# Kernel tuning notes

Hardware: AMD Instinct MI355X
Metric: run time of the kernel (lower is better)

Reference implementation:

```python
import jax, jax.numpy as jnp
import numpy as np

B, C, H, W = 8, 512, 64, 64
HN = 8
HD = C // HN


def setup_inputs() -> dict:
    key = jax.random.key(0)
    ks = jax.random.split(key, 10)
    s = lambda k, shape: jax.random.normal(k, shape, jnp.float32) * 0.02
    return dict(
        x_opt=jax.random.normal(ks[0], (B, C, H, W), jnp.float32),
        x_sar=jax.random.normal(ks[1], (B, C, H, W), jnp.float32),
        ln_o_w=jnp.ones((C,), jnp.float32), ln_o_b=jnp.zeros((C,), jnp.float32),
        ln_s_w=jnp.ones((C,), jnp.float32), ln_s_b=jnp.zeros((C,), jnp.float32),
        wq=s(ks[2], (C, C)), bq=jnp.zeros((C,), jnp.float32),
        wk=s(ks[3], (C, C)), bk=jnp.zeros((C,), jnp.float32),
        wv=s(ks[4], (C, C)), bv=jnp.zeros((C,), jnp.float32),
        w1=s(ks[5], (C, 2 * C)), b1=jnp.zeros((2 * C,), jnp.float32),
        w2=s(ks[6], (2 * C, C)), b2=jnp.zeros((C,), jnp.float32),
        wo=s(ks[7], (C, C)), bo=jnp.zeros((C,), jnp.float32),
    )


def _ln2d(x, w, b, eps=1e-5):
    # LayerNorm over channel dim of [B,C,H,W]
    m = x.mean(axis=1, keepdims=True)
    v = x.var(axis=1, keepdims=True)
    return (x - m) / jnp.sqrt(v + eps) * w[None, :, None, None] + b[None, :, None, None]


def _conv1x1(x, w, b):
    # 1x1 conv == per-pixel channel matmul; w: [out,in]
    return jnp.einsum('bchw,dc->bdhw', x, w) + b[None, :, None, None]


def reference(x_opt, x_sar, ln_o_w, ln_o_b, ln_s_w, ln_s_b,
              wq, bq, wk, bk, wv, bv, w1, b1, w2, b2, wo, bo):
    Bb, Cc, Hh, Ww = x_opt.shape
    HW = Hh * Ww
    xo = _ln2d(x_opt, ln_o_w, ln_o_b)
    xs = _ln2d(x_sar, ln_s_w, ln_s_b)
    q = _conv1x1(xo, wq, bq).reshape(Bb, HN, HD, HW)
    k = _conv1x1(xs, wk, bk).reshape(Bb, HN, HD, HW)
    v = _conv1x1(xs, wv, bv).reshape(Bb, HN, HD, HW).transpose(0, 1, 3, 2)  # [B,HN,HW,HD]
    # L2-normalize over the spatial (HW) axis, F.normalize eps semantics
    q = q / jnp.maximum(jnp.linalg.norm(q, axis=-1, keepdims=True), 1e-12)
    k = k / jnp.maximum(jnp.linalg.norm(k, axis=-1, keepdims=True), 1e-12)
    # channel-channel attention in fp32: [B,HN,HD,HD]
    attn = jnp.einsum('bhdn,bhen->bhde', q.astype(jnp.float32), k.astype(jnp.float32)) * (HD ** -0.5)
    attn = (attn - attn.max(axis=-1, keepdims=True)).astype(q.dtype)
    attn = jax.nn.softmax(attn, axis=-1)
    z = jnp.einsum('bhnd,bhde->bhne', v, attn)  # [B,HN,HW,HD]
    z = z.transpose(0, 2, 1, 3).reshape(Bb, HW, Cc)
    z_opt = xo.reshape(Bb, Cc, HW).transpose(0, 2, 1)
    z_sum = z + z_opt
    h = jax.nn.gelu(z_sum @ w1 + b1, approximate=False) @ w2 + b2
    z_out = (h + z_sum).transpose(0, 2, 1).reshape(Bb, Cc, Hh, Ww)
    z_out = _conv1x1(z_out, wo, bo)
    return xo + z_out
```

## Files before the change

### kernel.cpp

```cpp
#include <hip/hip_runtime.h>
#include <cstdint>
#include <cstddef>

#define DEVI __device__ __forceinline__

typedef __attribute__((ext_vector_type(8))) short short8;
typedef __attribute__((ext_vector_type(4))) float f32x4;
typedef __attribute__((ext_vector_type(2))) unsigned short u16x2;
typedef __attribute__((ext_vector_type(4))) unsigned short u16x4;
typedef __attribute__((ext_vector_type(8))) unsigned short u16x8;

#define Bn 8
#define Cn 512
#define HWn 4096
#define Mtot 32768

DEVI float b2f(unsigned short u) {
  union { uint32_t u; float f; } c; c.u = ((uint32_t)u) << 16; return c.f;
}
DEVI unsigned short f2b(float f) {
  union { float f; uint32_t u; } c; c.f = f;
  uint32_t u = c.u + 0x7fffu + ((c.u >> 16) & 1u);
  return (unsigned short)(u >> 16);
}
DEVI float gelu_fast(float x) {
  float y = 0.7978845608f * (x + 0.044715f * x * x * x);
  float e = __expf(2.0f * y);
  float t = 1.0f - 2.0f / (e + 1.0f);
  return 0.5f * x * (1.0f + t);
}

DEVI void async16(const void* g, void* l) {
  __builtin_amdgcn_global_load_lds((const __attribute__((address_space(1))) uint32_t*)g,
                                   (__attribute__((address_space(3))) uint32_t*)l, 16, 0, 0);
}

DEVI void stage128(const unsigned short* __restrict__ src, int ld, int row0, int kt,
                   char* lds, int t) {
  const int w = t >> 6;
  const int srow = t >> 3, sph = t & 7;
#pragma unroll
  for (int i = 0; i < 4; ++i) {
    int row = i * 32 + srow;
    int slog = sph ^ (row & 7);
    async16(src + (size_t)(row0 + row) * ld + kt + slog * 8, lds + i * 4096 + w * 1024);
  }
}

DEVI void stage256(const unsigned short* __restrict__ src, int ld, int row0, int kt,
                   char* lds, int t) {
  const int w = t >> 6;
  const int srow = t >> 3, sph = t & 7;
#pragma unroll
  for (int i = 0; i < 4; ++i) {
    int row = i * 64 + srow;
    int slog = sph ^ (row & 7);
    async16(src + (size_t)(row0 + row) * ld + kt + slog * 8, lds + i * 8192 + w * 1024);
  }
}

DEVI void gemm_compute(const unsigned short* As, const unsigned short* Bs,
                       int wr, int wc, int l15, int l4, f32x4 (&acc)[4][4]) {
#pragma unroll
  for (int ks = 0; ks < 2; ++ks) {
    short8 af[4], bfv[4];
#pragma unroll
    for (int m = 0; m < 4; ++m) {
      int row = wr * 64 + m * 16 + l15;
      int slog = ks * 4 + l4;
      af[m] = *(const short8*)&As[row * 64 + ((slog ^ (row & 7)) << 3)];
    }
#pragma unroll
    for (int n = 0; n < 4; ++n) {
      int row = wc * 64 + n * 16 + l15;
      int slog = ks * 4 + l4;
      bfv[n] = *(const short8*)&Bs[row * 64 + ((slog ^ (row & 7)) << 3)];
    }
#pragma unroll
    for (int m = 0; m < 4; ++m)
#pragma unroll
      for (int n = 0; n < 4; ++n)
        acc[m][n] = __builtin_amdgcn_mfma_f32_16x16x32_bf16(af[m], bfv[n], acc[m][n], 0, 0, 0);
  }
}

__global__ __launch_bounds__(256, 4) void k_qkv(
    const unsigned short* __restrict__ XO, const unsigned short* __restrict__ XS,
    const unsigned short* __restrict__ WQKV,
    const float* __restrict__ bq, const float* __restrict__ bk, const float* __restrict__ bv,
    unsigned short* __restrict__ Qb, unsigned short* __restrict__ KVb,
    float* __restrict__ sqQ, float* __restrict__ sqK) {
  __shared__ __align__(16) char smem[33792];
  unsigned short* As = (unsigned short*)smem;
  unsigned short* Bs = (unsigned short*)(smem + 16384);
  const int lin = blockIdx.x + 12 * blockIdx.y;
  const int xcd = lin & 7, j = lin >> 3;
  const int mt = xcd * 32 + j / 12;
  const int nt = j % 12;
  const int m0 = mt * 128, n0 = nt * 128;
  const unsigned short* A = (nt < 4) ? XO : XS;
  const float* bb = (nt < 4) ? (bq + n0) : (nt < 8 ? (bk + (nt - 4) * 128) : (bv + (nt - 8) * 128));
  float* sq = (nt < 4) ? sqQ : (nt < 8 ? sqK : nullptr);
  const int scol0 = (nt < 4) ? n0 : (nt - 4) * 128;
  unsigned short* ob = (nt < 4) ? Qb : KVb;
  const int ldo = (nt < 4) ? 512 : 1024;
  const int oc0 = (nt < 4) ? n0 : (nt - 4) * 128;
  const int t = threadIdx.x, w = t >> 6, lane = t & 63;
  const int wr = w >> 1, wc = w & 1, l15 = lane & 15, l4 = lane >> 4;
  f32x4 acc[4][4] = {};

  for (int kt = 0; kt < 512; kt += 64) {
    stage128(A, 512, m0, kt, (char*)As, t);
    stage128(WQKV, 512, n0, kt, (char*)Bs, t);
    __syncthreads();
    gemm_compute(As, Bs, wr, wc, l15, l4, acc);
    __syncthreads();
  }

  unsigned short* Cs = (unsigned short*)smem;
#pragma unroll
  for (int n = 0; n < 4; ++n) {
    int cn = wc * 64 + n * 16 + l15;
    float bn = bb[cn];
    float s2 = 0.f;
#pragma unroll
    for (int m = 0; m < 4; ++m) {
      int rb = wr * 64 + m * 16 + l4 * 4;
#pragma unroll
      for (int q = 0; q < 4; ++q) {
        float v = acc[m][n][q] + bn;
        s2 += v * v;
        Cs[(rb + q) * 132 + cn] = f2b(v);
      }
    }
    if (sq) {
      s2 += __shfl_xor(s2, 16, 64);
      s2 += __shfl_xor(s2, 32, 64);
      if (l4 == 0) atomicAdd(&sq[(m0 >> 12) * Cn + scol0 + cn], s2);
    }
  }
  __syncthreads();
#pragma unroll
  for (int pass = 0; pass < 4; ++pass) {
    int r = pass * 32 + (t >> 3);
    int c = (t & 7) * 8;
    u16x8 v0 = *(const u16x8*)&Cs[r * 132 + c];
    u16x8 v1 = *(const u16x8*)&Cs[r * 132 + 64 + c];
    size_t base = (size_t)(m0 + r) * ldo + oc0;
    *(u16x8*)&ob[base + c] = v0;
    *(u16x8*)&ob[base + 64 + c] = v1;
  }
}

template <int MODE>
__global__ __launch_bounds__(256, 4) void k_ffn(
    const unsigned short* __restrict__ A, const unsigned short* __restrict__ W,
    const float* __restrict__ bias, const unsigned short* __restrict__ res,
    unsigned short* __restrict__ out, int K, int N) {
  __shared__ __align__(16) char smem[33792];
  unsigned short* As = (unsigned short*)smem;
  unsigned short* Bs = (unsigned short*)(smem + 16384);
  const int NT = gridDim.x;
  const int lin = blockIdx.x + NT * blockIdx.y;
  const int xcd = lin & 7, j = lin >> 3;
  const int mt = xcd * 32 + j / NT;
  const int nt = j % NT;
  const int m0 = mt * 128, n0 = nt * 128;
  const int t = threadIdx.x, w = t >> 6, lane = t & 63;
  const int wr = w >> 1, wc = w & 1, l15 = lane & 15, l4 = lane >> 4;
  f32x4 acc[4][4] = {};

  for (int kt = 0; kt < K; kt += 64) {
    stage128(A, K, m0, kt, (char*)As, t);
    stage128(W, K, n0, kt, (char*)Bs, t);
    __syncthreads();
    gemm_compute(As, Bs, wr, wc, l15, l4, acc);
    __syncthreads();
  }

  unsigned short* Cs = (unsigned short*)smem;
#pragma unroll
  for (int n = 0; n < 4; ++n) {
    int cn = wc * 64 + n * 16 + l15;
    float bn = bias[n0 + cn];
#pragma unroll
    for (int m = 0; m < 4; ++m) {
      int rb = wr * 64 + m * 16 + l4 * 4;
#pragma unroll
      for (int q = 0; q < 4; ++q) {
        float v = acc[m][n][q] + bn;
        if (MODE == 1) v = gelu_fast(v);
        Cs[(rb + q) * 132 + cn] = f2b(v);
      }
    }
  }
  __syncthreads();
#pragma unroll
  for (int pass = 0; pass < 4; ++pass) {
    int r = pass * 32 + (t >> 3);
    int c = (t & 7) * 8;
    u16x8 v0 = *(const u16x8*)&Cs[r * 132 + c];
    u16x8 v1 = *(const u16x8*)&Cs[r * 132 + 64 + c];
    size_t base = (size_t)(m0 + r) * N + n0;
    if (MODE == 2) {
      u16x8 r0 = *(const u16x8*)&res[base + c];
      u16x8 r1 = *(const u16x8*)&res[base + 64 + c];
#pragma unroll
      for (int jj = 0; jj < 8; ++jj) {
        v0[jj] = f2b(b2f(v0[jj]) + b2f(r0[jj]));
        v1[jj] = f2b(b2f(v1[jj]) + b2f(r1[jj]));
      }
    }
    *(u16x8*)&out[base + c] = v0;
    *(u16x8*)&out[base + 64 + c] = v1;
  }
}

DEVI void compute256(const unsigned short* Ab, const unsigned short* Bb,
                     int wr, int wc, int l15, int l4, f32x4 (&acc)[8][4]) {
#pragma unroll
  for (int ks = 0; ks < 2; ++ks) {
    short8 aF[8], bF[4];
#pragma unroll
    for (int mf = 0; mf < 8; ++mf) {
      int row = wr * 128 + mf * 16 + l15;
      aF[mf] = *(const short8*)&Ab[row * 64 + (((ks * 4 + l4) ^ (row & 7)) << 3)];
    }
#pragma unroll
    for (int nf = 0; nf < 4; ++nf) {
      int row = wc * 64 + nf * 16 + l15;
      bF[nf] = *(const short8*)&Bb[row * 64 + (((ks * 4 + l4) ^ (row & 7)) << 3)];
    }
#pragma unroll
    for (int mf = 0; mf < 8; ++mf)
#pragma unroll
      for (int nf = 0; nf < 4; ++nf)
        acc[mf][nf] = __builtin_amdgcn_mfma_f32_16x16x32_bf16(aF[mf], bF[nf], acc[mf][nf], 0, 0, 0);
  }
}

__global__ __launch_bounds__(512, 2) void k_gemm_out(
    const unsigned short* __restrict__ Wo, const unsigned short* __restrict__ U,
    const float* __restrict__ bo, const float* __restrict__ xopt,
    const float* __restrict__ meanG, const float* __restrict__ rstdG,
    const float* __restrict__ lnw, const float* __restrict__ lnb,
    float* __restrict__ out) {
  __shared__ __align__(16) char smem[131072];
  const int lin = blockIdx.x;
  const int xcd = lin & 7, j = lin >> 3;
  const int b = xcd, mt = j & 1, nt = j >> 1;
  const int m0 = mt * 256, n0 = nt * 256;
  const unsigned short* Ub = U + (size_t)b * HWn * Cn;
  const int t = threadIdx.x, lane = t & 63;
  const int w = t >> 6, wr = w >> 2, wc = w & 3;
  const int l15 = lane & 15, l4 = lane >> 4;
  f32x4 acc[8][4] = {};

  stage256(Wo, 512, m0, 0, smem, t);
  stage256(Ub, 512, n0, 0, smem + 32768, t);
  __syncthreads();
  for (int kt = 0; kt < 8; ++kt) {
    if (kt + 1 < 8) {
      char* nb = smem + ((kt + 1) & 1) * 65536;
      stage256(Wo, 512, m0, (kt + 1) * 64, nb, t);
      stage256(Ub, 512, n0, (kt + 1) * 64, nb + 32768, t);
    }
    const unsigned short* Ab = (const unsigned short*)(smem + (kt & 1) * 65536);
    const unsigned short* Bb = (const unsigned short*)(smem + (kt & 1) * 65536 + 32768);
    compute256(Ab, Bb, wr, wc, l15, l4, acc);
    __syncthreads();
  }

  float* Fs = (float*)smem;
#pragma unroll
  for (int qd = 0; qd < 4; ++qd) {
    __syncthreads();
    if (wr == (qd >> 1)) {
#pragma unroll
      for (int nf = 0; nf < 4; ++nf) {
        int cn = wc * 64 + nf * 16 + l15;
#pragma unroll
        for (int mf2 = 0; mf2 < 4; ++mf2) {
          int mf = (qd & 1) * 4 + mf2;
#pragma unroll
          for (int q = 0; q < 4; ++q)
            Fs[(mf2 * 16 + l4 * 4 + q) * 260 + cn] = acc[mf][nf][q];
        }
      }
    }
    __syncthreads();
#pragma unroll
    for (int p = 0; p < 8; ++p) {
      int cl = p * 8 + w;
      int px = lane * 4;
      int c = m0 + qd * 64 + cl;
      size_t gbase = (size_t)(b * Cn + c) * HWn + n0 + px;
      f32x4 z = *(const f32x4*)&Fs[cl * 260 + px];
      f32x4 xv = *(const f32x4*)&xopt[gbase];
      f32x4 mn4 = *(const f32x4*)&meanG[b * HWn + n0 + px];
      f32x4 rs4 = *(const f32x4*)&rstdG[b * HWn + n0 + px];
      float lw = lnw[c], lb = lnb[c], bc = bo[c];
      f32x4 o;
#pragma unroll
      for (int jj = 0; jj < 4; ++jj)
        o[jj] = z[jj] + bc + (xv[jj] - mn4[jj]) * rs4[jj] * lw + lb;
      *(f32x4*)&out[gbase] = o;
    }
  }
}

__global__ __launch_bounds__(256, 2) void k_z(
    const unsigned short* __restrict__ V, int ldv, const unsigned short* __restrict__ PT,
    const unsigned short* __restrict__ XO, unsigned short* __restrict__ ZS) {
  __shared__ __align__(16) char smem[24576];
  unsigned short* As = (unsigned short*)smem;
  unsigned short* Bs = (unsigned short*)(smem + 16384);
  const int mt = blockIdx.x, bh = blockIdx.y, b = bh >> 3, h = bh & 7;
  const int t = threadIdx.x, w = t >> 6, lane = t & 63;
  const int wr = w >> 1, wc = w & 1, l15 = lane & 15, l4 = lane >> 4;
  const int srow = t >> 3, sph = t & 7;
#pragma unroll
  for (int i = 0; i < 4; ++i) {
    int row = i * 32 + srow;
    int slog = sph ^ (row & 7);
    async16(V + (size_t)(b * HWn + mt * 128 + row) * ldv + h * 64 + slog * 8,
            (char*)As + i * 4096 + w * 1024);
  }
#pragma unroll
  for (int i = 0; i < 2; ++i) {
    int row = i * 32 + srow;
    int slog = sph ^ (row & 7);
    async16(PT + (size_t)bh * 4096 + row * 64 + slog * 8, (char*)Bs + i * 4096 + w * 1024);
  }
  __syncthreads();
  f32x4 acc[4][2] = {};
#pragma unroll
  for (int ks = 0; ks < 2; ++ks) {
    short8 af[4], bfv[2];
#pragma unroll
    for (int m = 0; m < 4; ++m) {
      int row = wr * 64 + m * 16 + l15;
      int slog = ks * 4 + l4;
      af[m] = *(const short8*)&As[row * 64 + ((slog ^ (row & 7)) << 3)];
    }
#pragma unroll
    for (int n = 0; n < 2; ++n) {
      int row = wc * 32 + n * 16 + l15;
      int slog = ks * 4 + l4;
      bfv[n] = *(const short8*)&Bs[row * 64 + ((slog ^ (row & 7)) << 3)];
    }
#pragma unroll
    for (int m = 0; m < 4; ++m)
#pragma unroll
      for (int n = 0; n < 2; ++n)
        acc[m][n] = __builtin_amdgcn_mfma_f32_16x16x32_bf16(af[m], bfv[n], acc[m][n], 0, 0, 0);
  }
  __syncthreads();
  unsigned short* Cs = (unsigned short*)smem;
#pragma unroll
  for (int n = 0; n < 2; ++n) {
    int e = wc * 32 + n * 16 + l15;
#pragma unroll
    for (int m = 0; m < 4; ++m) {
      int rb = wr * 64 + m * 16 + l4 * 4;
#pragma unroll
      for (int q = 0; q < 4; ++q) Cs[(rb + q) * 72 + e] = f2b(acc[m][n][q]);
    }
  }
  __syncthreads();
#pragma unroll
  for (int pass = 0; pass < 4; ++pass) {
    int r = pass * 32 + (t >> 3);
    int c = (t & 7) * 8;
    u16x8 v = *(const u16x8*)&Cs[r * 72 + c];
    size_t idx = (size_t)(b * HWn + mt * 128 + r) * Cn + h * 64 + c;
    u16x8 xo = *(const u16x8*)&XO[idx];
#pragma unroll
    for (int jj = 0; jj < 8; ++jj) v[jj] = f2b(b2f(v[jj]) + b2f(xo[jj]));
    *(u16x8*)&ZS[idx] = v;
  }
}

__global__ __launch_bounds__(256, 2) void k_ln(
    const float* __restrict__ x_opt, const float* __restrict__ x_sar,
    const float* __restrict__ lwo, const float* __restrict__ lbo,
    const float* __restrict__ lws, const float* __restrict__ lbs,
    unsigned short* __restrict__ XO, unsigned short* __restrict__ XS,
    float* __restrict__ meanG, float* __restrict__ rstdG) {
  const int zz = blockIdx.z;
  const float* x = zz ? x_sar : x_opt;
  const float* lw = zz ? lws : lwo;
  const float* lb = zz ? lbs : lbo;
  unsigned short* out = zz ? XS : XO;
  __shared__ unsigned short stash[512 * 34];
  __shared__ float redS[256 * 4], redQ[256 * 4];
  __shared__ float meanS[32], rstdS[32], wS[512], bS[512];
  const int b = blockIdx.y, n0 = blockIdx.x * 32;
  const int t = threadIdx.x;
  wS[t] = lw[t]; wS[t + 256] = lw[t + 256];
  bS[t] = lb[t]; bS[t + 256] = lb[t + 256];
  const int cg = t >> 3, pq = t & 7;
  float sum[4] = {}, sq[4] = {};
  for (int r = 0; r < 16; ++r) {
    int c = r * 32 + cg;
    f32x4 v = *(const f32x4*)(x + (size_t)(b * Cn + c) * HWn + n0 + pq * 4);
#pragma unroll
    for (int j = 0; j < 4; ++j) { sum[j] += v[j]; sq[j] += v[j] * v[j]; }
    u16x2 h0 = {f2b(v[0]), f2b(v[1])};
    u16x2 h1 = {f2b(v[2]), f2b(v[3])};
    *(u16x2*)&stash[c * 34 + pq * 4] = h0;
    *(u16x2*)&stash[c * 34 + pq * 4 + 2] = h1;
  }
#pragma unroll
  for (int j = 0; j < 4; ++j) { redS[t * 4 + j] = sum[j]; redQ[t * 4 + j] = sq[j]; }
  __syncthreads();
  if (t < 32) {
    float s = 0.f, qq = 0.f;
    int pqq = t >> 2, j = t & 3;
    for (int g = 0; g < 32; ++g) {
      s += redS[(g * 8 + pqq) * 4 + j];
      qq += redQ[(g * 8 + pqq) * 4 + j];
    }
    float mean = s * (1.0f / 512.0f);
    float var = qq * (1.0f / 512.0f) - mean * mean;
    float rstd = rsqrtf(var + 1e-5f);
    meanS[t] = mean; rstdS[t] = rstd;
    if (!zz) { meanG[b * HWn + n0 + t] = mean; rstdG[b * HWn + n0 + t] = rstd; }
  }
  __syncthreads();
  const int p = t >> 3, cs = t & 7;
  float mn = meanS[p], rs = rstdS[p];
  for (int ch = 0; ch < 4; ++ch) {
    u16x8 o0, o1;
#pragma unroll
    for (int j = 0; j < 16; ++j) {
      int c = ch * 128 + cs * 16 + j;
      float xv = b2f(stash[c * 34 + p]);
      unsigned short r2 = f2b((xv - mn) * rs * wS[c] + bS[c]);
      if (j < 8) o0[j] = r2; else o1[j - 8] = r2;
    }
    size_t base = (size_t)(b * HWn + n0 + p) * Cn + ch * 128 + cs * 16;
    *(u16x8*)&out[base] = o0;
    *(u16x8*)&out[base + 8] = o1;
  }
}

__global__ __launch_bounds__(256, 2) void k_attn_part(
    const unsigned short* __restrict__ Q, int ldq,
    const unsigned short* __restrict__ Kb, int ldk,
    float* __restrict__ Praw) {
  __shared__ __align__(16) unsigned short QT[64 * 136];
  __shared__ __align__(16) unsigned short KT[64 * 136];
  const int bh = blockIdx.x, ns = blockIdx.y, b = bh >> 3, h = bh & 7;
  const int t = threadIdx.x, w = t >> 6, lane = t & 63;
  const int l15 = lane & 15, l4 = lane >> 4;
  const int dh = w >> 1, eh = w & 1;
  const int c8 = t >> 5, rr = t & 31;
  f32x4 acc[2][2] = {};
  for (int chunk = 0; chunk < 4; ++chunk) {
    int n0 = ns * 512 + chunk * 128;
    __syncthreads();
#pragma unroll
    for (int pass = 0; pass < 2; ++pass) {
      int row = n0 + pass * 64 + 2 * rr;
      u16x8 q0 = *(const u16x8*)(Q + (size_t)(b * HWn + row) * ldq + h * 64 + c8 * 8);
      u16x8 q1 = *(const u16x8*)(Q + (size_t)(b * HWn + row + 1) * ldq + h * 64 + c8 * 8);
      u16x8 k0 = *(const u16x8*)(Kb + (size_t)(b * HWn + row) * ldk + h * 64 + c8 * 8);
      u16x8 k1 = *(const u16x8*)(Kb + (size_t)(b * HWn + row + 1) * ldk + h * 64 + c8 * 8);
#pragma unroll
      for (int j = 0; j < 8; ++j) {
        u16x2 pq = {q0[j], q1[j]};
        u16x2 pk = {k0[j], k1[j]};
        *(u16x2*)&QT[(c8 * 8 + j) * 136 + pass * 64 + 2 * rr] = pq;
        *(u16x2*)&KT[(c8 * 8 + j) * 136 + pass * 64 + 2 * rr] = pk;
      }
    }
    __syncthreads();
#pragma unroll
    for (int ks = 0; ks < 4; ++ks) {
      short8 af[2], bfv[2];
#pragma unroll
      for (int m = 0; m < 2; ++m)
        af[m] = *(const short8*)&QT[(dh * 32 + m * 16 + l15) * 136 + ks * 32 + l4 * 8];
#pragma unroll
      for (int n = 0; n < 2; ++n)
        bfv[n] = *(const short8*)&KT[(eh * 32 + n * 16 + l15) * 136 + ks * 32 + l4 * 8];
#pragma unroll
      for (int m = 0; m < 2; ++m)
#pragma unroll
        for (int n = 0; n < 2; ++n)
          acc[m][n] = __builtin_amdgcn_mfma_f32_16x16x32_bf16(af[m], bfv[n], acc[m][n], 0, 0, 0);
    }
  }
#pragma unroll
  for (int m = 0; m < 2; ++m)
#pragma unroll
    for (int n = 0; n < 2; ++n)
#pragma unroll
      for (int q = 0; q < 4; ++q) {
        int dd = dh * 32 + m * 16 + l4 * 4 + q;
        int ee = eh * 32 + n * 16 + l15;
        atomicAdd(&Praw[(size_t)bh * 4096 + dd * 64 + ee], acc[m][n][q]);
      }
}

__global__ __launch_bounds__(256, 2) void k_softmax(
    const float* __restrict__ Praw, const float* __restrict__ sqQ,
    const float* __restrict__ sqK, unsigned short* __restrict__ PT) {
  __shared__ float P3[64 * 66];
  const int bh = blockIdx.x, b = bh >> 3, h = bh & 7;
  const int t = threadIdx.x, w = t >> 6, lane = t & 63;
  float rk = 1.0f / fmaxf(sqrtf(sqK[b * Cn + h * 64 + lane]), 1e-12f);
  for (int i = 0; i < 16; ++i) {
    int d = w * 16 + i;
    float rqd = 1.0f / fmaxf(sqrtf(sqQ[b * Cn + h * 64 + d]), 1e-12f);
    float v = Praw[(size_t)bh * 4096 + d * 64 + lane] * (rqd * rk * 0.125f);
    float m = v;
    for (int o = 32; o > 0; o >>= 1) m = fmaxf(m, __shfl_xor(m, o, 64));
    float p = __expf(v - m);
    float s = p;
    for (int o = 32; o > 0; o >>= 1) s += __shfl_xor(s, o, 64);
    P3[lane * 66 + d] = p / s;
  }
  __syncthreads();
  {
    int e = t >> 2, dg = (t & 3) * 16;
    u16x8 o0, o1;
#pragma unroll
    for (int j = 0; j < 8; ++j) {
      o0[j] = f2b(P3[e * 66 + dg + j]);
      o1[j] = f2b(P3[e * 66 + dg + 8 + j]);
    }
    size_t base = (size_t)bh * 4096 + e * 64 + dg;
    *(u16x8*)&PT[base] = o0;
    *(u16x8*)&PT[base + 8] = o1;
  }
}

__global__ void k_prep(const float* __restrict__ wq, const float* __restrict__ wk,
                       const float* __restrict__ wv, const float* __restrict__ wo,
                       const float* __restrict__ w1, const float* __restrict__ w2,
                       unsigned short* __restrict__ WQKV, unsigned short* __restrict__ WO,
                       unsigned short* __restrict__ W1T, unsigned short* __restrict__ W2T) {
  int bid = blockIdx.x;
  if (bid < 1024) {
    const int mat = bid >> 8, chunk = bid & 255;
    const float* s = mat == 0 ? wq : mat == 1 ? wk : mat == 2 ? wv : wo;
    unsigned short* d = mat == 3 ? WO : (WQKV + mat * 262144);
    int idx = chunk * 1024 + threadIdx.x * 4;
    f32x4 v = *(const f32x4*)(s + idx);
    u16x4 o = {f2b(v[0]), f2b(v[1]), f2b(v[2]), f2b(v[3])};
    *(u16x4*)(d + idx) = o;
    return;
  }
  bid -= 1024;
  __shared__ float tile[32][33];
  const float* src; unsigned short* dst; int R, C, r0, c0;
  if (bid < 512) { src = w1; dst = W1T; R = 512; C = 1024; r0 = (bid >> 5) * 32; c0 = (bid & 31) * 32; }
  else { bid -= 512; src = w2; dst = W2T; R = 1024; C = 512; r0 = (bid >> 4) * 32; c0 = (bid & 15) * 32; }
  const int tx = threadIdx.x & 31, ty = threadIdx.x >> 5;
#pragma unroll
  for (int i = 0; i < 4; ++i)
    tile[ty + i * 8][tx] = src[(size_t)(r0 + ty + i * 8) * C + c0 + tx];
  __syncthreads();
#pragma unroll
  for (int i = 0; i < 4; ++i)
    dst[(size_t)(c0 + ty + i * 8) * R + r0 + tx] = f2b(tile[tx][ty + i * 8]);
}

extern "C" void kernel_launch(void* const* d_in, const int* in_sizes, int n_in,
                              void* d_out, int out_size, void* d_ws, size_t ws_size,
                              hipStream_t stream) {
  const float* x_opt = (const float*)d_in[0];
  const float* x_sar = (const float*)d_in[1];
  const float* ln_o_w = (const float*)d_in[2];
  const float* ln_o_b = (const float*)d_in[3];
  const float* ln_s_w = (const float*)d_in[4];
  const float* ln_s_b = (const float*)d_in[5];
  const float* wq = (const float*)d_in[6];
  const float* bq = (const float*)d_in[7];
  const float* wk = (const float*)d_in[8];
  const float* bk = (const float*)d_in[9];
  const float* wv = (const float*)d_in[10];
  const float* bv = (const float*)d_in[11];
  const float* w1 = (const float*)d_in[12];
  const float* b1 = (const float*)d_in[13];
  const float* w2 = (const float*)d_in[14];
  const float* b2 = (const float*)d_in[15];
  const float* wo = (const float*)d_in[16];
  const float* bo = (const float*)d_in[17];
  float* out = (float*)d_out;

  char* ws = (char*)d_ws;
  const size_t S = (size_t)Mtot * Cn * 2;
  unsigned short* XO = (unsigned short*)(ws);
  unsigned short* XS = (unsigned short*)(ws + S);
  unsigned short* Qb = (unsigned short*)(ws + 2 * S);
  unsigned short* KVb = (unsigned short*)(ws + 3 * S);
  unsigned short* ZS = (unsigned short*)(ws + 5 * S);
  unsigned short* H1 = Qb;
  unsigned short* Ub = XS;
  char* E = ws + 6 * S;
  unsigned short* PT = (unsigned short*)(E);
  float* Praw = (float*)(E + 524288);
  float* sqQ = (float*)(E + 524288 + 1048576);
  float* sqK = (float*)(E + 524288 + 1048576 + 16384);
  float* meanG = (float*)(E + 524288 + 1048576 + 32768);
  float* rstdG = (float*)(E + 524288 + 1048576 + 32768 + 131072);
  char* Wb = E + 1867776;
  unsigned short* WQKV = (unsigned short*)(Wb);
  unsigned short* WO = (unsigned short*)(Wb + 1572864);
  unsigned short* W1T = (unsigned short*)(Wb + 2097152);
  unsigned short* W2T = (unsigned short*)(Wb + 2097152 + 1048576);

  hipMemsetAsync(E + 524288, 0, 1048576 + 32768, stream);

  k_prep<<<2048, 256, 0, stream>>>(wq, wk, wv, wo, w1, w2, WQKV, WO, W1T, W2T);

  k_ln<<<dim3(128, Bn, 2), 256, 0, stream>>>(x_opt, x_sar, ln_o_w, ln_o_b, ln_s_w, ln_s_b,
                                             XO, XS, meanG, rstdG);

  k_qkv<<<dim3(12, 256), 256, 0, stream>>>(XO, XS, WQKV, bq, bk, bv, Qb, KVb, sqQ, sqK);

  k_attn_part<<<dim3(64, 8), 256, 0, stream>>>(Qb, 512, KVb, 1024, Praw);
  k_softmax<<<64, 256, 0, stream>>>(Praw, sqQ, sqK, PT);
  k_z<<<dim3(32, 64), 256, 0, stream>>>(KVb + 512, 1024, PT, XO, ZS);

  k_ffn<1><<<dim3(8, 256), 256, 0, stream>>>(ZS, W1T, b1, nullptr, H1, 512, 1024);
  k_ffn<2><<<dim3(4, 256), 256, 0, stream>>>(H1, W2T, b2, ZS, Ub, 1024, 512);
  k_gemm_out<<<256, 512, 0, stream>>>(WO, Ub, bo, x_opt, meanG, rstdG,
                                      ln_o_w, ln_o_b, out);
}
```

Measured before the change: 303.0 us.

## Widen QKV and FFN GEMM tiles to 128x256 with 512-thread blocks

Merges the QKV projection and the two FFN GEMMs into one templated kernel that computes 128x256 output tiles with 8 waves instead of 128x128 with 4 waves. Each A tile is now reused across twice as many output columns, which cuts global and LDS loads per FLOP. The epilogue writes through LDS in two halves and keeps the per-mode bias, GELU, residual and squared-norm atomics. The cost is more LDS per block (48KB) and half as many blocks, which may lower occupancy and leave the GPU less full.

New measurement: 344.5 us. 1.14x slower.

```diff
diff --git a/kernel.cpp b/kernel.cpp
--- a/kernel.cpp
+++ b/kernel.cpp
@@ -35,6 +35,17 @@
                                    (__attribute__((address_space(3))) uint32_t*)l, 16, 0, 0);
 }
 
+DEVI void stageN(const unsigned short* __restrict__ src, int ld, int row0, int kt,
+                 char* lds, int t, int passes) {
+  const int w = t >> 6;
+  const int srow = t >> 3, sph = t & 7;
+  for (int i = 0; i < passes; ++i) {
+    int row = i * 64 + srow;
+    int slog = sph ^ (row & 7);
+    async16(src + (size_t)(row0 + row) * ld + kt + slog * 8, lds + i * 8192 + w * 1024);
+  }
+}
+
 DEVI void stage128(const unsigned short* __restrict__ src, int ld, int row0, int kt,
                    char* lds, int t) {
   const int w = t >> 6;
@@ -47,18 +58,6 @@
   }
 }
 
-DEVI void stage256(const unsigned short* __restrict__ src, int ld, int row0, int kt,
-                   char* lds, int t) {
-  const int w = t >> 6;
-  const int srow = t >> 3, sph = t & 7;
-#pragma unroll
-  for (int i = 0; i < 4; ++i) {
-    int row = i * 64 + srow;
-    int slog = sph ^ (row & 7);
-    async16(src + (size_t)(row0 + row) * ld + kt + slog * 8, lds + i * 8192 + w * 1024);
-  }
-}
-
 DEVI void gemm_compute(const unsigned short* As, const unsigned short* Bs,
                        int wr, int wc, int l15, int l4, f32x4 (&acc)[4][4]) {
 #pragma unroll
@@ -84,34 +83,31 @@
   }
 }
 
-__global__ __launch_bounds__(256, 4) void k_qkv(
-    const unsigned short* __restrict__ XO, const unsigned short* __restrict__ XS,
-    const unsigned short* __restrict__ WQKV,
-    const float* __restrict__ bq, const float* __restrict__ bk, const float* __restrict__ bv,
-    unsigned short* __restrict__ Qb, unsigned short* __restrict__ KVb,
-    float* __restrict__ sqQ, float* __restrict__ sqK) {
-  __shared__ __align__(16) char smem[33792];
+template <int MODE>
+__global__ __launch_bounds__(512, 4) void k_gw(
+    const unsigned short* __restrict__ A, const unsigned short* __restrict__ A2,
+    const unsigned short* __restrict__ W,
+    const float* __restrict__ bias, const float* __restrict__ bias2,
+    const float* __restrict__ bias3, const unsigned short* __restrict__ res,
+    unsigned short* __restrict__ out, unsigned short* __restrict__ out2,
+    int K, int N, float* __restrict__ sqQ, float* __restrict__ sqK) {
+  __shared__ __align__(16) char smem[49152];
   unsigned short* As = (unsigned short*)smem;
   unsigned short* Bs = (unsigned short*)(smem + 16384);
-  const int lin = blockIdx.x + 12 * blockIdx.y;
+  const int NT2 = gridDim.x;
+  const int lin = blockIdx.x + NT2 * blockIdx.y;
   const int xcd = lin & 7, j = lin >> 3;
-  const int mt = xcd * 32 + j / 12;
-  const int nt = j % 12;
-  const int m0 = mt * 128, n0 = nt * 128;
-  const unsigned short* A = (nt < 4) ? XO : XS;
-  const float* bb = (nt < 4) ? (bq + n0) : (nt < 8 ? (bk + (nt - 4) * 128) : (bv + (nt - 8) * 128));
-  float* sq = (nt < 4) ? sqQ : (nt < 8 ? sqK : nullptr);
-  const int scol0 = (nt < 4) ? n0 : (nt - 4) * 128;
-  unsigned short* ob = (nt < 4) ? Qb : KVb;
-  const int ldo = (nt < 4) ? 512 : 1024;
-  const int oc0 = (nt < 4) ? n0 : (nt - 4) * 128;
+  const int mt = xcd * 32 + j / NT2;
+  const int nt2 = j % NT2;
+  const int m0 = mt * 128, n0 = nt2 * 256;
+  const unsigned short* Ag = (MODE == 0 && nt2 >= 2) ? A2 : A;
   const int t = threadIdx.x, w = t >> 6, lane = t & 63;
-  const int wr = w >> 1, wc = w & 1, l15 = lane & 15, l4 = lane >> 4;
+  const int wr = w >> 2, wc = w & 3, l15 = lane & 15, l4 = lane >> 4;
   f32x4 acc[4][4] = {};
 
-  for (int kt = 0; kt < 512; kt += 64) {
-    stage128(A, 512, m0, kt, (char*)As, t);
-    stage128(WQKV, 512, n0, kt, (char*)Bs, t);
+  for (int kt = 0; kt < K; kt += 64) {
+    stageN(Ag, K, m0, kt, (char*)As, t, 2);
+    stageN(W, K, n0, kt, (char*)Bs, t, 4);
     __syncthreads();
     gemm_compute(As, Bs, wr, wc, l15, l4, acc);
     __syncthreads();
@@ -119,100 +115,60 @@
 
   unsigned short* Cs = (unsigned short*)smem;
 #pragma unroll
-  for (int n = 0; n < 4; ++n) {
-    int cn = wc * 64 + n * 16 + l15;
-    float bn = bb[cn];
-    float s2 = 0.f;
-#pragma unroll
-    for (int m = 0; m < 4; ++m) {
-      int rb = wr * 64 + m * 16 + l4 * 4;
-#pragma unroll
-      for (int q = 0; q < 4; ++q) {
-        float v = acc[m][n][q] + bn;
-        s2 += v * v;
-        Cs[(rb + q) * 132 + cn] = f2b(v);
+  for (int hh = 0; hh < 2; ++hh) {
+    __syncthreads();
+    if ((wc >> 1) == hh) {
+#pragma unroll
+      for (int n = 0; n < 4; ++n) {
+        int cnl = (wc & 1) * 64 + n * 16 + l15;
+        int colg = n0 + hh * 128 + cnl;
+        float bn;
+        if (MODE == 0)
+          bn = (colg < 512) ? bias[colg] : (colg < 1024 ? bias2[colg - 512] : bias3[colg - 1024]);
+        else
+          bn = bias[colg];
+        float s2 = 0.f;
+#pragma unroll
+        for (int m = 0; m < 4; ++m) {
+          int rb = wr * 64 + m * 16 + l4 * 4;
+#pragma unroll
+          for (int q = 0; q < 4; ++q) {
+            float v = acc[m][n][q] + bn;
+            if (MODE == 1) v = gelu_fast(v);
+            if (MODE == 0) s2 += v * v;
+            Cs[(rb + q) * 132 + cnl] = f2b(v);
+          }
+        }
+        if (MODE == 0 && colg < 1024) {
+          float* sq = (colg < 512) ? sqQ : sqK;
+          s2 += __shfl_xor(s2, 16, 64);
+          s2 += __shfl_xor(s2, 32, 64);
+          if (l4 == 0) atomicAdd(&sq[(m0 >> 12) * Cn + (colg & 511)], s2);
+        }
       }
     }
-    if (sq) {
-      s2 += __shfl_xor(s2, 16, 64);
-      s2 += __shfl_xor(s2, 32, 64);
-      if (l4 == 0) atomicAdd(&sq[(m0 >> 12) * Cn + scol0 + cn], s2);
-    }
-  }
-  __syncthreads();
-#pragma unroll
-  for (int pass = 0; pass < 4; ++pass) {
-    int r = pass * 32 + (t >> 3);
-    int c = (t & 7) * 8;
-    u16x8 v0 = *(const u16x8*)&Cs[r * 132 + c];
-    u16x8 v1 = *(const u16x8*)&Cs[r * 132 + 64 + c];
-    size_t base = (size_t)(m0 + r) * ldo + oc0;
-    *(u16x8*)&ob[base + c] = v0;
-    *(u16x8*)&ob[base + 64 + c] = v1;
-  }
-}
-
-template <int MODE>
-__global__ __launch_bounds__(256, 4) void k_ffn(
-    const unsigned short* __restrict__ A, const unsigned short* __restrict__ W,
-    const float* __restrict__ bias, const unsigned short* __restrict__ res,
-    unsigned short* __restrict__ out, int K, int N) {
-  __shared__ __align__(16) char smem[33792];
-  unsigned short* As = (unsigned short*)smem;
-  unsigned short* Bs = (unsigned short*)(smem + 16384);
-  const int NT = gridDim.x;
-  const int lin = blockIdx.x + NT * blockIdx.y;
-  const int xcd = lin & 7, j = lin >> 3;
-  const int mt = xcd * 32 + j / NT;
-  const int nt = j % NT;
-  const int m0 = mt * 128, n0 = nt * 128;
-  const int t = threadIdx.x, w = t >> 6, lane = t & 63;
-  const int wr = w >> 1, wc = w & 1, l15 = lane & 15, l4 = lane >> 4;
-  f32x4 acc[4][4] = {};
-
-  for (int kt = 0; kt < K; kt += 64) {
-    stage128(A, K, m0, kt, (char*)As, t);
-    stage128(W, K, n0, kt, (char*)Bs, t);
-    __syncthreads();
-    gemm_compute(As, Bs, wr, wc, l15, l4, acc);
-    __syncthreads();
-  }
-
-  unsigned short* Cs = (unsigned short*)smem;
-#pragma unroll
-  for (int n = 0; n < 4; ++n) {
-    int cn = wc * 64 + n * 16 + l15;
-    float bn = bias[n0 + cn];
-#pragma unroll
-    for (int m = 0; m < 4; ++m) {
-      int rb = wr * 64 + m * 16 + l4 * 4;
-#pragma unroll
-      for (int q = 0; q < 4; ++q) {
-        float v = acc[m][n][q] + bn;
-        if (MODE == 1) v = gelu_fast(v);
-        Cs[(rb + q) * 132 + cn] = f2b(v);
+    __syncthreads();
+    int r = t >> 2, c = (t & 3) * 32;
+    int colg0 = n0 + hh * 128 + c;
+    unsigned short* ob;
+    size_t base;
+    if (MODE == 0) {
+      if (colg0 < 512) { ob = out; base = (size_t)(m0 + r) * 512 + colg0; }
+      else { ob = out2; base = (size_t)(m0 + r) * 1024 + (colg0 - 512); }
+    } else {
+      ob = out;
+      base = (size_t)(m0 + r) * N + colg0;
+    }
+#pragma unroll
+    for (int u = 0; u < 4; ++u) {
+      u16x8 v = *(const u16x8*)&Cs[r * 132 + c + u * 8];
+      if (MODE == 2) {
+        u16x8 rv = *(const u16x8*)&res[base + u * 8];
+#pragma unroll
+        for (int jj = 0; jj < 8; ++jj) v[jj] = f2b(b2f(v[jj]) + b2f(rv[jj]));
       }
-    }
-  }
-  __syncthreads();
-#pragma unroll
-  for (int pass = 0; pass < 4; ++pass) {
-    int r = pass * 32 + (t >> 3);
-    int c = (t & 7) * 8;
-    u16x8 v0 = *(const u16x8*)&Cs[r * 132 + c];
-    u16x8 v1 = *(const u16x8*)&Cs[r * 132 + 64 + c];
-    size_t base = (size_t)(m0 + r) * N + n0;
-    if (MODE == 2) {
-      u16x8 r0 = *(const u16x8*)&res[base + c];
-      u16x8 r1 = *(const u16x8*)&res[base + 64 + c];
-#pragma unroll
-      for (int jj = 0; jj < 8; ++jj) {
-        v0[jj] = f2b(b2f(v0[jj]) + b2f(r0[jj]));
-        v1[jj] = f2b(b2f(v1[jj]) + b2f(r1[jj]));
-      }
-    }
-    *(u16x8*)&out[base + c] = v0;
-    *(u16x8*)&out[base + 64 + c] = v1;
+      *(u16x8*)&ob[base + u * 8] = v;
+    }
   }
 }
 
@@ -256,14 +212,14 @@
   const int l15 = lane & 15, l4 = lane >> 4;
   f32x4 acc[8][4] = {};
 
-  stage256(Wo, 512, m0, 0, smem, t);
-  stage256(Ub, 512, n0, 0, smem + 32768, t);
+  stageN(Wo, 512, m0, 0, smem, t, 4);
+  stageN(Ub, 512, n0, 0, smem + 32768, t, 4);
   __syncthreads();
   for (int kt = 0; kt < 8; ++kt) {
     if (kt + 1 < 8) {
       char* nb = smem + ((kt + 1) & 1) * 65536;
-      stage256(Wo, 512, m0, (kt + 1) * 64, nb, t);
-      stage256(Ub, 512, n0, (kt + 1) * 64, nb + 32768, t);
+      stageN(Wo, 512, m0, (kt + 1) * 64, nb, t, 4);
+      stageN(Ub, 512, n0, (kt + 1) * 64, nb + 32768, t, 4);
     }
     const unsigned short* Ab = (const unsigned short*)(smem + (kt & 1) * 65536);
     const unsigned short* Bb = (const unsigned short*)(smem + (kt & 1) * 65536 + 32768);
@@ -620,14 +576,17 @@
   k_ln<<<dim3(128, Bn, 2), 256, 0, stream>>>(x_opt, x_sar, ln_o_w, ln_o_b, ln_s_w, ln_s_b,
                                              XO, XS, meanG, rstdG);
 
-  k_qkv<<<dim3(12, 256), 256, 0, stream>>>(XO, XS, WQKV, bq, bk, bv, Qb, KVb, sqQ, sqK);
+  k_gw<0><<<dim3(6, 256), 512, 0, stream>>>(XO, XS, WQKV, bq, bk, bv, nullptr,
+                                            Qb, KVb, 512, 1536, sqQ, sqK);
 
   k_attn_part<<<dim3(64, 8), 256, 0, stream>>>(Qb, 512, KVb, 1024, Praw);
   k_softmax<<<64, 256, 0, stream>>>(Praw, sqQ, sqK, PT);
   k_z<<<dim3(32, 64), 256, 0, stream>>>(KVb + 512, 1024, PT, XO, ZS);
 
-  k_ffn<1><<<dim3(8, 256), 256, 0, stream>>>(ZS, W1T, b1, nullptr, H1, 512, 1024);
-  k_ffn<2><<<dim3(4, 256), 256, 0, stream>>>(H1, W2T, b2, ZS, Ub, 1024, 512);
+  k_gw<1><<<dim3(4, 256), 512, 0, stream>>>(ZS, nullptr, W1T, b1, nullptr, nullptr, nullptr,
+                                            H1, nullptr, 512, 1024, nullptr, nullptr);
+  k_gw<2><<<dim3(2, 256), 512, 0, stream>>>(H1, nullptr, W2T, b2, nullptr, nullptr, ZS,
+                                            Ub, nullptr, 1024, 512, nullptr, nullptr);
   k_gemm_out<<<256, 512, 0, stream>>>(WO, Ub, bo, x_opt, meanG, rstdG,
                                       ln_o_w, ln_o_b, out);
 }
```
